# Kernel optimization log

Measured on AMD Instinct MI355X. Metric: run time of the kernel, lower is better.

Reference implementation:

```python
import jax, jax.numpy as jnp
import numpy as np

B, S, HID = 2, 2048, 2048
H, HKV = 16, 4
D = HID // H          # 128
N_REP = H // HKV      # 4
ROPE_THETA = 1000000.0


def _rope_tables(seq_len, head_dim, theta):
    inv_freq = 1.0 / (theta ** (jnp.arange(0, head_dim, 2, dtype=jnp.float32) / head_dim))
    freqs = jnp.arange(seq_len, dtype=jnp.float32)[:, None] * inv_freq[None, :]  # [S, D/2]
    emb = jnp.concatenate([freqs, freqs], axis=-1)  # [S, D]
    return jnp.cos(emb), jnp.sin(emb)


def setup_inputs() -> dict:
    key = jax.random.key(0)
    ks = jax.random.split(key, 6)
    cos, sin = _rope_tables(S, D, ROPE_THETA)
    sc = 0.02
    return {
        "x": jax.random.normal(ks[0], (B, S, HID), jnp.float32),
        "cos": cos,
        "sin": sin,
        "Wq": jax.random.normal(ks[1], (HID, H * D), jnp.float32) * sc,
        "Wk": jax.random.normal(ks[2], (HID, HKV * D), jnp.float32) * sc,
        "Wv": jax.random.normal(ks[3], (HID, HKV * D), jnp.float32) * sc,
        "Wo": jax.random.normal(ks[4], (H * D, HID), jnp.float32) * sc,
    }


def _rotate_half(t):
    t1, t2 = jnp.split(t, 2, axis=-1)
    return jnp.concatenate([-t2, t1], axis=-1)


def reference(x, cos, sin, Wq, Wk, Wv, Wo):
    b, s, _ = x.shape
    q = (x @ Wq).reshape(b, s, H, D)    # [b,s,H,d]
    k = (x @ Wk).reshape(b, s, HKV, D)  # [b,s,Hkv,d]
    v = (x @ Wv).reshape(b, s, HKV, D)

    # RoPE (cos/sin broadcast over head axis)
    c = cos[:s, None, :]  # [s,1,d]
    sn = sin[:s, None, :]
    q = q * c + _rotate_half(q) * sn
    k = k * c + _rotate_half(k) * sn

    # GQA: repeat kv heads (interleaved, matching repeat_kv)
    k = jnp.repeat(k, N_REP, axis=2)  # [b,s,H,d]
    v = jnp.repeat(v, N_REP, axis=2)

    q = q.transpose(0, 2, 1, 3)  # [b,H,s,d]
    k = k.transpose(0, 2, 1, 3)
    v = v.transpose(0, 2, 1, 3)

    scale = 1.0 / jnp.sqrt(jnp.asarray(D, x.dtype))
    scores = jnp.einsum("bhqd,bhkd->bhqk", q, k) * scale
    causal = jnp.tril(jnp.ones((s, s), dtype=bool))
    scores = jnp.where(causal[None, None], scores, jnp.asarray(-jnp.inf, scores.dtype))
    probs = jax.nn.softmax(scores, axis=-1)
    out = jnp.einsum("bhqk,bhkd->bhqd", probs, v)
    out = out.transpose(0, 2, 1, 3).reshape(b, s, H * D)
    return out @ Wo
```

## Files before the change

kernel.cpp:

```cpp
#include <hip/hip_runtime.h>
#include <cstdint>

#define B_    2
#define S_    2048
#define HID_  2048
#define H_    16
#define HKV_  4
#define D_    128
#define SCALE_ 0.08838834764831845f
#define LOG2E_ 1.4426950408889634f
#define K1_   (SCALE_ * LOG2E_)
#define THRS_ 62.75f

typedef __bf16 bf16x8 __attribute__((ext_vector_type(8)));
typedef float  f32x4  __attribute__((ext_vector_type(4)));
typedef int    intx2  __attribute__((ext_vector_type(2)));
using u16 = unsigned short;

static __device__ __forceinline__ u16 f2bf(float f) {
  union { float f; uint32_t u; } c; c.f = f;
  uint32_t u = c.u;
  return (u16)((u + 0x7FFFu + ((u >> 16) & 1u)) >> 16);
}
static __device__ __forceinline__ float bf2f(u16 h) {
  union { uint32_t u; float f; } c; c.u = ((uint32_t)h) << 16;
  return c.f;
}
static __device__ __forceinline__ void async16(const u16* g, u16* lds) {
  __builtin_amdgcn_global_load_lds((const __attribute__((address_space(1))) void*)g,
                                   (__attribute__((address_space(3))) void*)lds, 16, 0, 0);
}

__global__ void cast_f32_bf16(const float* __restrict__ in, u16* __restrict__ out, int n4) {
  int i = blockIdx.x * blockDim.x + threadIdx.x;
  if (i < n4) {
    float4 v = ((const float4*)in)[i];
    ushort4 o;
    o.x = f2bf(v.x); o.y = f2bf(v.y); o.z = f2bf(v.z); o.w = f2bf(v.w);
    ((ushort4*)out)[i] = o;
  }
}

__global__ __launch_bounds__(256) void transpose_cast_all(const float* __restrict__ Wq,
                                                          const float* __restrict__ Wk,
                                                          const float* __restrict__ Wv,
                                                          const float* __restrict__ Wo,
                                                          u16* __restrict__ Wt,
                                                          u16* __restrict__ Wot) {
  __shared__ float tile[32][33];
  const int tx = threadIdx.x, ty = threadIdx.y;
  const int t = blockIdx.x;
  const float* W; u16* Dst; int N, lt;
  if (t < 4096)      { W = Wq; Dst = Wt;                        N = 2048; lt = t; }
  else if (t < 5120) { W = Wk; Dst = Wt + (size_t)2048 * 2048;  N = 512;  lt = t - 4096; }
  else if (t < 6144) { W = Wv; Dst = Wt + (size_t)2560 * 2048;  N = 512;  lt = t - 5120; }
  else               { W = Wo; Dst = Wot;                       N = 2048; lt = t - 6144; }
  const int tn = N >> 5;
  const int n0 = (lt % tn) * 32, k0 = (lt / tn) * 32;
#pragma unroll
  for (int j = 0; j < 32; j += 8)
    tile[ty + j][tx] = W[(size_t)(k0 + ty + j) * N + n0 + tx];
  __syncthreads();
#pragma unroll
  for (int j = 0; j < 32; j += 8)
    Dst[(size_t)(n0 + ty + j) * 2048 + k0 + tx] = f2bf(tile[tx][ty + j]);
}

__global__ __launch_bounds__(256) void v_transpose(const u16* __restrict__ qkv,
                                                   u16* __restrict__ Vt) {
  __shared__ u16 tile[32][34];
  const int tx = threadIdx.x, ty = threadIdx.y;
  const int mat = blockIdx.z;
  const int b = mat >> 2, kv = mat & 3;
  const int d0 = blockIdx.x * 32, s0 = blockIdx.y * 32;
#pragma unroll
  for (int j = 0; j < 32; j += 8)
    tile[ty + j][tx] = qkv[(size_t)(b * S_ + s0 + ty + j) * 3072 + 2560 + kv * 128 + d0 + tx];
  __syncthreads();
#pragma unroll
  for (int j = 0; j < 32; j += 8)
    Vt[((size_t)mat * D_ + d0 + ty + j) * S_ + s0 + tx] = tile[tx][ty + j];
}

template<int BF16OUT>
__global__ __launch_bounds__(256, 4) void gemm_bt(const u16* __restrict__ A,
                                                  const u16* __restrict__ Bt,
                                                  void* __restrict__ Cv,
                                                  int M, int N, int K, int gx) {
  const int nwg = (int)gridDim.x;
  const int bid = (int)blockIdx.x;
  const int qq = nwg >> 3, rr = nwg & 7;
  const int xcd = bid & 7, pos = bid >> 3;
  const int wg = ((xcd < rr) ? xcd * (qq + 1) : rr * (qq + 1) + (xcd - rr) * qq) + pos;
  const int bm = (wg % gx) * 128;
  const int bn = (wg / gx) * 128;

  __shared__ __align__(16) u16 Ash[128 * 64];
  __shared__ __align__(16) u16 Bsh[128 * 64];
  const int tid = threadIdx.x;
  const int w = tid >> 6, l = tid & 63;
  const int wm = (w >> 1) * 64, wn = (w & 1) * 64;

  const f32x4 z4 = {0.f, 0.f, 0.f, 0.f};
  f32x4 acc[4][4];
#pragma unroll
  for (int i = 0; i < 4; ++i)
#pragma unroll
    for (int j = 0; j < 4; ++j) acc[i][j] = z4;

  const int srow = w * 8 + (l >> 3);
  const int schunk = l & 7;

  for (int k0 = 0; k0 < K; k0 += 64) {
#pragma unroll
    for (int i = 0; i < 4; ++i) {
      const int row = i * 32 + srow;
      const int ch = schunk ^ (row & 7);
      async16(A + (size_t)(bm + row) * K + k0 + ch * 8, &Ash[(i * 4 + w) * 512]);
      async16(Bt + (size_t)(bn + row) * K + k0 + ch * 8, &Bsh[(i * 4 + w) * 512]);
    }
    asm volatile("s_waitcnt vmcnt(0)" ::: "memory");
    __syncthreads();
#pragma unroll
    for (int kc = 0; kc < 2; ++kc) {
      bf16x8 af[4], bfr[4];
#pragma unroll
      for (int mi = 0; mi < 4; ++mi) {
        const int r = wm + mi * 16 + (l & 15);
        const int c2 = (kc * 4 + (l >> 4)) ^ (r & 7);
        af[mi] = *(const bf16x8*)&Ash[r * 64 + c2 * 8];
      }
#pragma unroll
      for (int ni = 0; ni < 4; ++ni) {
        const int r = wn + ni * 16 + (l & 15);
        const int c2 = (kc * 4 + (l >> 4)) ^ (r & 7);
        bfr[ni] = *(const bf16x8*)&Bsh[r * 64 + c2 * 8];
      }
#pragma unroll
      for (int mi = 0; mi < 4; ++mi)
#pragma unroll
        for (int ni = 0; ni < 4; ++ni)
          acc[mi][ni] = __builtin_amdgcn_mfma_f32_16x16x32_bf16(af[mi], bfr[ni], acc[mi][ni], 0, 0, 0);
    }
    __syncthreads();
  }
#pragma unroll
  for (int mi = 0; mi < 4; ++mi) {
    const int r0 = bm + wm + mi * 16 + ((l >> 4) << 2);
#pragma unroll
    for (int ni = 0; ni < 4; ++ni) {
      const int c = bn + wn + ni * 16 + (l & 15);
#pragma unroll
      for (int j = 0; j < 4; ++j) {
        if (BF16OUT) ((u16*)Cv)[(size_t)(r0 + j) * N + c] = f2bf(acc[mi][ni][j]);
        else         ((float*)Cv)[(size_t)(r0 + j) * N + c] = acc[mi][ni][j];
      }
    }
  }
}

__global__ void rope_scatter(const u16* __restrict__ qkv,
                             const float* __restrict__ cosb, const float* __restrict__ sinb,
                             u16* __restrict__ Qr, u16* __restrict__ Kr) {
  const int NQ = B_ * S_ * H_ * 64;
  const int NK = B_ * S_ * HKV_ * 64;
  const int idx = blockIdx.x * 256 + threadIdx.x;
  if (idx < NQ) {
    const int j = idx & 63, rest = idx >> 6;
    const int h = rest & 15, srow = rest >> 4;
    const int s = srow & (S_ - 1);
    const u16* base = qkv + (size_t)srow * 3072 + h * 128;
    const float c = cosb[s * 128 + j], sn = sinb[s * 128 + j];
    const float a = bf2f(base[j]), b2 = bf2f(base[j + 64]);
    const size_t qo = (((size_t)(srow >> 11) * H_ + h) * S_ + s) * D_;
    Qr[qo + j]      = f2bf(a * c - b2 * sn);
    Qr[qo + j + 64] = f2bf(b2 * c + a * sn);
  } else if (idx < NQ + NK) {
    const int t = idx - NQ;
    const int j = t & 63, rest = t >> 6;
    const int kv = rest & 3, srow = rest >> 2;
    const int s = srow & (S_ - 1);
    const u16* base = qkv + (size_t)srow * 3072 + 2048 + kv * 128;
    const float c = cosb[s * 128 + j], sn = sinb[s * 128 + j];
    const float a = bf2f(base[j]), b2 = bf2f(base[j + 64]);
    const size_t ko = (((size_t)(srow >> 11) * HKV_ + kv) * S_ + s) * D_;
    Kr[ko + j]      = f2bf(a * c - b2 * sn);
    Kr[ko + j + 64] = f2bf(b2 * c + a * sn);
  }
}

__global__ __launch_bounds__(256, 2) void attn_kernel(const u16* __restrict__ Q,
                                                      const u16* __restrict__ Kc,
                                                      const u16* __restrict__ Vt,
                                                      u16* __restrict__ O) {
  const int bid = blockIdx.x;
  const int bh  = bid & 31;
  const int qt  = (bid < 256) ? (15 - ((bid >> 5) & 7)) : ((bid >> 5) & 7);
  const int b   = bh >> 4;
  const int kvh = (bh & 15) >> 2;
  const int tid = threadIdx.x;
  const int w = tid >> 6, l = tid & 63;
  const int g = l >> 4, c = l & 15;
  const int q0 = qt * 128;

  __shared__ __align__(16) u16 KshF[2 * 64 * 128];
  __shared__ __align__(16) u16 VshF[2 * 128 * 64];

  const u16* Kbase = Kc + ((size_t)(b * HKV_ + kvh) * S_) * D_;
  const u16* Vbase = Vt + ((size_t)(b * HKV_ + kvh) * D_) * S_;

  bf16x8 qf[2][4];
#pragma unroll
  for (int qg = 0; qg < 2; ++qg) {
    const u16* qp = Q + ((size_t)bh * S_ + q0 + w * 32 + qg * 16 + c) * D_ + g * 8;
#pragma unroll
    for (int kc = 0; kc < 4; ++kc) qf[qg][kc] = *(const bf16x8*)(qp + kc * 32);
  }

  int srcK[4], srcV[4];
#pragma unroll
  for (int i = 0; i < 4; ++i) {
    const int rK = i * 16 + w * 4 + g;
    srcK[i] = rK * 128 + (c ^ (rK & 7)) * 8;
    const int dV = i * 32 + w * 8 + (l >> 3);
    srcV[i] = dV * S_ + ((l & 7) ^ (dV & 7)) * 8;
  }

  const f32x4 z4 = {0.f, 0.f, 0.f, 0.f};
  f32x4 oacc[2][8];
#pragma unroll
  for (int qg = 0; qg < 2; ++qg)
#pragma unroll
    for (int nb = 0; nb < 8; ++nb) oacc[qg][nb] = z4;
  float m_i[2] = {-1e30f, -1e30f}, l_i[2] = {0.f, 0.f};

  auto stage = [&](int buf, int kv0) {
#pragma unroll
    for (int i = 0; i < 4; ++i) {
      async16(Kbase + (size_t)kv0 * 128 + srcK[i], &KshF[buf * 8192 + i * 2048 + w * 512]);
      async16(Vbase + kv0 + srcV[i],               &VshF[buf * 8192 + i * 2048 + w * 512]);
    }
  };

  const uint32_t voff = (uint32_t)(c * 128 + (((g >> 1) ^ (c & 7)) << 4) + ((g & 1) << 3));

  const int nt = (q0 + 128) >> 6;
  stage(0, 0);
  __syncthreads();

  for (int t = 0; t < nt; ++t) {
    const int cur = t & 1;
    const int kv0 = t << 6;
    if (t + 1 < nt) stage(cur ^ 1, (t + 1) << 6);

    if (kv0 <= q0 + w * 32 + 31) {
      const u16*  Kb = &KshF[cur * 8192];
      const char* Vb = (const char*)&VshF[cur * 8192];

      f32x4 sf[2][4];
#pragma unroll
      for (int qg = 0; qg < 2; ++qg)
#pragma unroll
        for (int nb = 0; nb < 4; ++nb) sf[qg][nb] = z4;

      __builtin_amdgcn_s_setprio(1);
#pragma unroll
      for (int kc = 0; kc < 4; ++kc) {
#pragma unroll
        for (int nb = 0; nb < 4; ++nb) {
          const int r = nb * 16 + c;
          const int s2 = (kc * 4 + g) ^ (c & 7);
          const bf16x8 kf = *(const bf16x8*)&Kb[r * 128 + s2 * 8];
          sf[0][nb] = __builtin_amdgcn_mfma_f32_16x16x32_bf16(kf, qf[0][kc], sf[0][nb], 0, 0, 0);
          sf[1][nb] = __builtin_amdgcn_mfma_f32_16x16x32_bf16(kf, qf[1][kc], sf[1][nb], 0, 0, 0);
        }
      }
      __builtin_amdgcn_s_setprio(0);

#pragma unroll
      for (int qg = 0; qg < 2; ++qg) {
        const int qcol = q0 + w * 32 + qg * 16 + c;
        const bool doMask = (kv0 + 63 > q0 + w * 32 + qg * 16);
        float mx = -3e38f;
#pragma unroll
        for (int nb = 0; nb < 4; ++nb)
#pragma unroll
          for (int jj = 0; jj < 4; ++jj) {
            float sv = sf[qg][nb][jj];
            if (doMask) {
              const int kk = kv0 + nb * 16 + g * 4 + jj;
              sv = (kk > qcol) ? -3e38f : sv;
              sf[qg][nb][jj] = sv;
            }
            mx = fmaxf(mx, sv);
          }
        mx = fmaxf(mx, __shfl_xor(mx, 16));
        mx = fmaxf(mx, __shfl_xor(mx, 32));

        if (__all(mx <= m_i[qg] + THRS_)) {
          const float mk = m_i[qg] * K1_;
          float rs = 0.f;
#pragma unroll
          for (int nb = 0; nb < 4; ++nb)
#pragma unroll
            for (int jj = 0; jj < 4; ++jj) {
              const float p = exp2f(fmaf(sf[qg][nb][jj], K1_, -mk));
              sf[qg][nb][jj] = p;
              rs += p;
            }
          rs += __shfl_xor(rs, 16);
          rs += __shfl_xor(rs, 32);
          l_i[qg] += rs;
        } else {
          const float mnew = fmaxf(m_i[qg], mx);
          const float fsc = exp2f((m_i[qg] - mnew) * K1_);
          m_i[qg] = mnew;
          const float mk = mnew * K1_;
          float rs = 0.f;
#pragma unroll
          for (int nb = 0; nb < 4; ++nb)
#pragma unroll
            for (int jj = 0; jj < 4; ++jj) {
              const float p = exp2f(fmaf(sf[qg][nb][jj], K1_, -mk));
              sf[qg][nb][jj] = p;
              rs += p;
            }
          rs += __shfl_xor(rs, 16);
          rs += __shfl_xor(rs, 32);
          l_i[qg] = l_i[qg] * fsc + rs;
          float fq[4];
#pragma unroll
          for (int j = 0; j < 4; ++j) fq[j] = __shfl(fsc, g * 4 + j);
#pragma unroll
          for (int nb = 0; nb < 8; ++nb)
#pragma unroll
            for (int j = 0; j < 4; ++j) oacc[qg][nb][j] *= fq[j];
        }
      }

      bf16x8 paq0, paq1, pbq0, pbq1;
#pragma unroll
      for (int jj = 0; jj < 4; ++jj) {
        paq0[jj] = (__bf16)sf[0][0][jj]; paq0[4 + jj] = (__bf16)sf[0][1][jj];
        pbq0[jj] = (__bf16)sf[0][2][jj]; pbq0[4 + jj] = (__bf16)sf[0][3][jj];
        paq1[jj] = (__bf16)sf[1][0][jj]; paq1[4 + jj] = (__bf16)sf[1][1][jj];
        pbq1[jj] = (__bf16)sf[1][2][jj]; pbq1[4 + jj] = (__bf16)sf[1][3][jj];
      }

      __builtin_amdgcn_s_setprio(1);
#pragma unroll
      for (int kc2 = 0; kc2 < 2; ++kc2) {
        const bf16x8 pa0 = kc2 ? pbq0 : paq0;
        const bf16x8 pa1 = kc2 ? pbq1 : paq1;
        const uint32_t vk = voff ^ (uint32_t)(kc2 << 6);
#pragma unroll
        for (int nb = 0; nb < 8; ++nb) {
          union { intx2 h[2]; bf16x8 v; } u_;
          u_.h[0] = *(const intx2*)(Vb + (vk + nb * 2048));
          u_.h[1] = *(const intx2*)(Vb + ((vk ^ 32u) + nb * 2048));
          oacc[0][nb] = __builtin_amdgcn_mfma_f32_16x16x32_bf16(pa0, u_.v, oacc[0][nb], 0, 0, 0);
          oacc[1][nb] = __builtin_amdgcn_mfma_f32_16x16x32_bf16(pa1, u_.v, oacc[1][nb], 0, 0, 0);
        }
      }
      __builtin_amdgcn_s_setprio(0);
    }

    __syncthreads();
  }

#pragma unroll
  for (int qg = 0; qg < 2; ++qg)
#pragma unroll
    for (int j = 0; j < 4; ++j) {
      const float li = __shfl(l_i[qg], g * 4 + j);
      const float inv = 1.f / li;
      const int srow = q0 + w * 32 + qg * 16 + g * 4 + j;
      u16* op = O + ((size_t)(b * S_ + srow)) * HID_ + (bh & 15) * D_ + c;
#pragma unroll
      for (int nb = 0; nb < 8; ++nb) op[nb * 16] = f2bf(oacc[qg][nb][j] * inv);
    }
}

extern "C" void kernel_launch(void* const* d_in, const int* in_sizes, int n_in,
                              void* d_out, int out_size, void* d_ws, size_t ws_size,
                              hipStream_t stream) {
  const float* x    = (const float*)d_in[0];
  const float* cosb = (const float*)d_in[1];
  const float* sinb = (const float*)d_in[2];
  const float* Wq   = (const float*)d_in[3];
  const float* Wk   = (const float*)d_in[4];
  const float* Wv   = (const float*)d_in[5];
  const float* Wo   = (const float*)d_in[6];
  float* out = (float*)d_out;

  u16*   xb   = (u16*)d_ws;
  u16*   Wt   = xb  + (size_t)4096 * 2048;
  u16*   Wot  = Wt  + (size_t)3072 * 2048;
  u16*   qkv  = Wot + (size_t)2048 * 2048;
  u16*   Qr   = qkv + (size_t)4096 * 3072;
  u16*   Kr   = Qr  + (size_t)B_ * H_ * S_ * D_;
  u16*   Vtb  = Kr  + (size_t)B_ * HKV_ * S_ * D_;
  u16*   Ob   = Vtb + (size_t)B_ * HKV_ * S_ * D_;

  cast_f32_bf16<<<8192, 256, 0, stream>>>(x, xb, (B_ * S_ * HID_) / 4);

  dim3 tb(32, 8);
  transpose_cast_all<<<dim3(10240), tb, 0, stream>>>(Wq, Wk, Wv, Wo, Wt, Wot);

  gemm_bt<1><<<dim3(768), 256, 0, stream>>>(xb, Wt, qkv, 4096, 3072, 2048, 32);

  rope_scatter<<<20480, 256, 0, stream>>>(qkv, cosb, sinb, Qr, Kr);
  v_transpose<<<dim3(4, 64, 8), tb, 0, stream>>>(qkv, Vtb);

  attn_kernel<<<dim3(512), 256, 0, stream>>>(Qr, Kr, Vtb, Ob);

  gemm_bt<0><<<dim3(512), 256, 0, stream>>>(Ob, Wot, out, 4096, 2048, 2048, 32);
}
```

Measured before the change: 232.2 us.

## Halve attention query tile to 64 rows, single-buffer K/V, raise occupancy

The attention kernel now processes 64 query rows per block (16 per wave) instead of 128, launches 1024 blocks in longest-first order, and requests 4 blocks per CU. K/V staging drops from double-buffered async prefetch to a single buffer with a wait and barrier every tile. The aim is more parallelism and occupancy from smaller register and LDS footprints. In exchange each K/V tile is loaded twice as often across blocks, and load latency is no longer overlapped with compute inside a block, so it relies on other resident blocks to hide it.

```diff
diff --git a/kernel.cpp b/kernel.cpp
--- a/kernel.cpp
+++ b/kernel.cpp
@@ -189,32 +189,31 @@
   }
 }
 
-__global__ __launch_bounds__(256, 2) void attn_kernel(const u16* __restrict__ Q,
+__global__ __launch_bounds__(256, 4) void attn_kernel(const u16* __restrict__ Q,
                                                       const u16* __restrict__ Kc,
                                                       const u16* __restrict__ Vt,
                                                       u16* __restrict__ O) {
   const int bid = blockIdx.x;
   const int bh  = bid & 31;
-  const int qt  = (bid < 256) ? (15 - ((bid >> 5) & 7)) : ((bid >> 5) & 7);
+  const int qt  = 31 - (bid >> 5);
   const int b   = bh >> 4;
   const int kvh = (bh & 15) >> 2;
   const int tid = threadIdx.x;
   const int w = tid >> 6, l = tid & 63;
   const int g = l >> 4, c = l & 15;
-  const int q0 = qt * 128;
-
-  __shared__ __align__(16) u16 KshF[2 * 64 * 128];
-  __shared__ __align__(16) u16 VshF[2 * 128 * 64];
+  const int q0 = qt * 64;
+
+  __shared__ __align__(16) u16 Ksh[64 * 128];
+  __shared__ __align__(16) u16 Vsh[128 * 64];
 
   const u16* Kbase = Kc + ((size_t)(b * HKV_ + kvh) * S_) * D_;
   const u16* Vbase = Vt + ((size_t)(b * HKV_ + kvh) * D_) * S_;
 
-  bf16x8 qf[2][4];
-#pragma unroll
-  for (int qg = 0; qg < 2; ++qg) {
-    const u16* qp = Q + ((size_t)bh * S_ + q0 + w * 32 + qg * 16 + c) * D_ + g * 8;
-#pragma unroll
-    for (int kc = 0; kc < 4; ++kc) qf[qg][kc] = *(const bf16x8*)(qp + kc * 32);
+  bf16x8 qf[4];
+  {
+    const u16* qp = Q + ((size_t)bh * S_ + q0 + w * 16 + c) * D_ + g * 8;
+#pragma unroll
+    for (int kc = 0; kc < 4; ++kc) qf[kc] = *(const bf16x8*)(qp + kc * 32);
   }
 
   int srcK[4], srcV[4];
@@ -227,158 +226,138 @@
   }
 
   const f32x4 z4 = {0.f, 0.f, 0.f, 0.f};
-  f32x4 oacc[2][8];
-#pragma unroll
-  for (int qg = 0; qg < 2; ++qg)
-#pragma unroll
-    for (int nb = 0; nb < 8; ++nb) oacc[qg][nb] = z4;
-  float m_i[2] = {-1e30f, -1e30f}, l_i[2] = {0.f, 0.f};
-
-  auto stage = [&](int buf, int kv0) {
+  f32x4 oacc[8];
+#pragma unroll
+  for (int nb = 0; nb < 8; ++nb) oacc[nb] = z4;
+  float m_i = -1e30f, l_i = 0.f;
+
+  auto stage = [&](int kv0) {
 #pragma unroll
     for (int i = 0; i < 4; ++i) {
-      async16(Kbase + (size_t)kv0 * 128 + srcK[i], &KshF[buf * 8192 + i * 2048 + w * 512]);
-      async16(Vbase + kv0 + srcV[i],               &VshF[buf * 8192 + i * 2048 + w * 512]);
+      async16(Kbase + (size_t)kv0 * 128 + srcK[i], &Ksh[i * 2048 + w * 512]);
+      async16(Vbase + kv0 + srcV[i],               &Vsh[i * 2048 + w * 512]);
     }
   };
 
   const uint32_t voff = (uint32_t)(c * 128 + (((g >> 1) ^ (c & 7)) << 4) + ((g & 1) << 3));
 
-  const int nt = (q0 + 128) >> 6;
-  stage(0, 0);
-  __syncthreads();
-
+  const int nt = qt + 1;
   for (int t = 0; t < nt; ++t) {
-    const int cur = t & 1;
     const int kv0 = t << 6;
-    if (t + 1 < nt) stage(cur ^ 1, (t + 1) << 6);
-
-    if (kv0 <= q0 + w * 32 + 31) {
-      const u16*  Kb = &KshF[cur * 8192];
-      const char* Vb = (const char*)&VshF[cur * 8192];
-
-      f32x4 sf[2][4];
-#pragma unroll
-      for (int qg = 0; qg < 2; ++qg)
-#pragma unroll
-        for (int nb = 0; nb < 4; ++nb) sf[qg][nb] = z4;
-
-      __builtin_amdgcn_s_setprio(1);
-#pragma unroll
-      for (int kc = 0; kc < 4; ++kc) {
-#pragma unroll
-        for (int nb = 0; nb < 4; ++nb) {
-          const int r = nb * 16 + c;
-          const int s2 = (kc * 4 + g) ^ (c & 7);
-          const bf16x8 kf = *(const bf16x8*)&Kb[r * 128 + s2 * 8];
-          sf[0][nb] = __builtin_amdgcn_mfma_f32_16x16x32_bf16(kf, qf[0][kc], sf[0][nb], 0, 0, 0);
-          sf[1][nb] = __builtin_amdgcn_mfma_f32_16x16x32_bf16(kf, qf[1][kc], sf[1][nb], 0, 0, 0);
+    if (t) __syncthreads();
+    stage(kv0);
+    asm volatile("s_waitcnt vmcnt(0)" ::: "memory");
+    __syncthreads();
+
+    f32x4 sf[4];
+#pragma unroll
+    for (int nb = 0; nb < 4; ++nb) sf[nb] = z4;
+
+    __builtin_amdgcn_s_setprio(1);
+#pragma unroll
+    for (int kc = 0; kc < 4; ++kc) {
+#pragma unroll
+      for (int nb = 0; nb < 4; ++nb) {
+        const int r = nb * 16 + c;
+        const int s2 = (kc * 4 + g) ^ (c & 7);
+        const bf16x8 kf = *(const bf16x8*)&Ksh[r * 128 + s2 * 8];
+        sf[nb] = __builtin_amdgcn_mfma_f32_16x16x32_bf16(kf, qf[kc], sf[nb], 0, 0, 0);
+      }
+    }
+    __builtin_amdgcn_s_setprio(0);
+
+    {
+      const int qcol = q0 + w * 16 + c;
+      const bool doMask = (t == nt - 1);
+      float mx = -3e38f;
+#pragma unroll
+      for (int nb = 0; nb < 4; ++nb)
+#pragma unroll
+        for (int jj = 0; jj < 4; ++jj) {
+          float sv = sf[nb][jj];
+          if (doMask) {
+            const int kk = kv0 + nb * 16 + g * 4 + jj;
+            sv = (kk > qcol) ? -3e38f : sv;
+            sf[nb][jj] = sv;
+          }
+          mx = fmaxf(mx, sv);
         }
-      }
-      __builtin_amdgcn_s_setprio(0);
-
-#pragma unroll
-      for (int qg = 0; qg < 2; ++qg) {
-        const int qcol = q0 + w * 32 + qg * 16 + c;
-        const bool doMask = (kv0 + 63 > q0 + w * 32 + qg * 16);
-        float mx = -3e38f;
+      mx = fmaxf(mx, __shfl_xor(mx, 16));
+      mx = fmaxf(mx, __shfl_xor(mx, 32));
+
+      if (__all(mx <= m_i + THRS_)) {
+        const float mk = m_i * K1_;
+        float rs = 0.f;
 #pragma unroll
         for (int nb = 0; nb < 4; ++nb)
 #pragma unroll
           for (int jj = 0; jj < 4; ++jj) {
-            float sv = sf[qg][nb][jj];
-            if (doMask) {
-              const int kk = kv0 + nb * 16 + g * 4 + jj;
-              sv = (kk > qcol) ? -3e38f : sv;
-              sf[qg][nb][jj] = sv;
-            }
-            mx = fmaxf(mx, sv);
+            const float p = exp2f(fmaf(sf[nb][jj], K1_, -mk));
+            sf[nb][jj] = p;
+            rs += p;
           }
-        mx = fmaxf(mx, __shfl_xor(mx, 16));
-        mx = fmaxf(mx, __shfl_xor(mx, 32));
-
-        if (__all(mx <= m_i[qg] + THRS_)) {
-          const float mk = m_i[qg] * K1_;
-          float rs = 0.f;
-#pragma unroll
-          for (int nb = 0; nb < 4; ++nb)
-#pragma unroll
-            for (int jj = 0; jj < 4; ++jj) {
-              const float p = exp2f(fmaf(sf[qg][nb][jj], K1_, -mk));
-              sf[qg][nb][jj] = p;
-              rs += p;
-            }
-          rs += __shfl_xor(rs, 16);
-          rs += __shfl_xor(rs, 32);
-          l_i[qg] += rs;
-        } else {
-          const float mnew = fmaxf(m_i[qg], mx);
-          const float fsc = exp2f((m_i[qg] - mnew) * K1_);
-          m_i[qg] = mnew;
-          const float mk = mnew * K1_;
-          float rs = 0.f;
-#pragma unroll
-          for (int nb = 0; nb < 4; ++nb)
-#pragma unroll
-            for (int jj = 0; jj < 4; ++jj) {
-              const float p = exp2f(fmaf(sf[qg][nb][jj], K1_, -mk));
-              sf[qg][nb][jj] = p;
-              rs += p;
-            }
-          rs += __shfl_xor(rs, 16);
-          rs += __shfl_xor(rs, 32);
-          l_i[qg] = l_i[qg] * fsc + rs;
-          float fq[4];
-#pragma unroll
-          for (int j = 0; j < 4; ++j) fq[j] = __shfl(fsc, g * 4 + j);
-#pragma unroll
-          for (int nb = 0; nb < 8; ++nb)
-#pragma unroll
-            for (int j = 0; j < 4; ++j) oacc[qg][nb][j] *= fq[j];
-        }
-      }
-
-      bf16x8 paq0, paq1, pbq0, pbq1;
-#pragma unroll
-      for (int jj = 0; jj < 4; ++jj) {
-        paq0[jj] = (__bf16)sf[0][0][jj]; paq0[4 + jj] = (__bf16)sf[0][1][jj];
-        pbq0[jj] = (__bf16)sf[0][2][jj]; pbq0[4 + jj] = (__bf16)sf[0][3][jj];
-        paq1[jj] = (__bf16)sf[1][0][jj]; paq1[4 + jj] = (__bf16)sf[1][1][jj];
-        pbq1[jj] = (__bf16)sf[1][2][jj]; pbq1[4 + jj] = (__bf16)sf[1][3][jj];
-      }
-
-      __builtin_amdgcn_s_setprio(1);
-#pragma unroll
-      for (int kc2 = 0; kc2 < 2; ++kc2) {
-        const bf16x8 pa0 = kc2 ? pbq0 : paq0;
-        const bf16x8 pa1 = kc2 ? pbq1 : paq1;
-        const uint32_t vk = voff ^ (uint32_t)(kc2 << 6);
-#pragma unroll
-        for (int nb = 0; nb < 8; ++nb) {
-          union { intx2 h[2]; bf16x8 v; } u_;
-          u_.h[0] = *(const intx2*)(Vb + (vk + nb * 2048));
-          u_.h[1] = *(const intx2*)(Vb + ((vk ^ 32u) + nb * 2048));
-          oacc[0][nb] = __builtin_amdgcn_mfma_f32_16x16x32_bf16(pa0, u_.v, oacc[0][nb], 0, 0, 0);
-          oacc[1][nb] = __builtin_amdgcn_mfma_f32_16x16x32_bf16(pa1, u_.v, oacc[1][nb], 0, 0, 0);
-        }
-      }
-      __builtin_amdgcn_s_setprio(0);
-    }
-
-    __syncthreads();
-  }
-
-#pragma unroll
-  for (int qg = 0; qg < 2; ++qg)
-#pragma unroll
-    for (int j = 0; j < 4; ++j) {
-      const float li = __shfl(l_i[qg], g * 4 + j);
-      const float inv = 1.f / li;
-      const int srow = q0 + w * 32 + qg * 16 + g * 4 + j;
-      u16* op = O + ((size_t)(b * S_ + srow)) * HID_ + (bh & 15) * D_ + c;
-#pragma unroll
-      for (int nb = 0; nb < 8; ++nb) op[nb * 16] = f2bf(oacc[qg][nb][j] * inv);
-    }
+        rs += __shfl_xor(rs, 16);
+        rs += __shfl_xor(rs, 32);
+        l_i += rs;
+      } else {
+        const float mnew = fmaxf(m_i, mx);
+        const float fsc = exp2f((m_i - mnew) * K1_);
+        m_i = mnew;
+        const float mk = mnew * K1_;
+        float rs = 0.f;
+#pragma unroll
+        for (int nb = 0; nb < 4; ++nb)
+#pragma unroll
+          for (int jj = 0; jj < 4; ++jj) {
+            const float p = exp2f(fmaf(sf[nb][jj], K1_, -mk));
+            sf[nb][jj] = p;
+            rs += p;
+          }
+        rs += __shfl_xor(rs, 16);
+        rs += __shfl_xor(rs, 32);
+        l_i = l_i * fsc + rs;
+        float fq[4];
+#pragma unroll
+        for (int j = 0; j < 4; ++j) fq[j] = __shfl(fsc, g * 4 + j);
+#pragma unroll
+        for (int nb = 0; nb < 8; ++nb)
+#pragma unroll
+          for (int j = 0; j < 4; ++j) oacc[nb][j] *= fq[j];
+      }
+    }
+
+    bf16x8 pa, pb;
+#pragma unroll
+    for (int jj = 0; jj < 4; ++jj) {
+      pa[jj] = (__bf16)sf[0][jj]; pa[4 + jj] = (__bf16)sf[1][jj];
+      pb[jj] = (__bf16)sf[2][jj]; pb[4 + jj] = (__bf16)sf[3][jj];
+    }
+
+    __builtin_amdgcn_s_setprio(1);
+#pragma unroll
+    for (int kc2 = 0; kc2 < 2; ++kc2) {
+      const bf16x8 pfr = kc2 ? pb : pa;
+      const uint32_t vk = voff ^ (uint32_t)(kc2 << 6);
+#pragma unroll
+      for (int nb = 0; nb < 8; ++nb) {
+        union { intx2 h[2]; bf16x8 v; } u_;
+        u_.h[0] = *(const intx2*)((const char*)Vsh + (vk + nb * 2048));
+        u_.h[1] = *(const intx2*)((const char*)Vsh + ((vk ^ 32u) + nb * 2048));
+        oacc[nb] = __builtin_amdgcn_mfma_f32_16x16x32_bf16(pfr, u_.v, oacc[nb], 0, 0, 0);
+      }
+    }
+    __builtin_amdgcn_s_setprio(0);
+  }
+
+#pragma unroll
+  for (int j = 0; j < 4; ++j) {
+    const float li = __shfl(l_i, g * 4 + j);
+    const float inv = 1.f / li;
+    const int srow = q0 + w * 16 + g * 4 + j;
+    u16* op = O + ((size_t)(b * S_ + srow)) * HID_ + (bh & 15) * D_ + c;
+#pragma unroll
+    for (int nb = 0; nb < 8; ++nb) op[nb * 16] = f2bf(oacc[nb][j] * inv);
+  }
 }
 
 extern "C" void kernel_launch(void* const* d_in, const int* in_sizes, int n_in,
@@ -412,7 +391,7 @@
   rope_scatter<<<20480, 256, 0, stream>>>(qkv, cosb, sinb, Qr, Kr);
   v_transpose<<<dim3(4, 64, 8), tb, 0, stream>>>(qkv, Vtb);
 
-  attn_kernel<<<dim3(512), 256, 0, stream>>>(Qr, Kr, Vtb, Ob);
+  attn_kernel<<<dim3(1024), 256, 0, stream>>>(Qr, Kr, Vtb, Ob);
 
   gemm_bt<0><<<dim3(512), 256, 0, stream>>>(Ob, Wot, out, 4096, 2048, 2048, 32);
 }
```

Measured after the change: 283.7 us. +22.2%, slower.
